# Performance work log

Measured on AMD Instinct MI355X. Metric: run time of the kernel, lower is better.

## Reference

```python
import jax, jax.numpy as jnp
import numpy as np

# Sparse grid constants (closed over; coords live on this grid)
B, H, W = 2, 640, 640
N = 409600
CIN, CH, COUT = 64, 64, 64
K = 3
PAD = (K - 1) // 2


def setup_inputs() -> dict:
    key = jax.random.key(0)
    ks = jax.random.split(key, 6)
    # unique active coordinates via permutation of the dense grid
    lin = jax.random.permutation(ks[0], B * H * W)[:N]
    b = lin // (H * W)
    rem = lin % (H * W)
    coords = jnp.stack([b, rem // W, rem % W], axis=1).astype(jnp.int32)  # [N,3]
    features = jax.random.normal(ks[1], (N, CIN), jnp.float32)
    w1 = jax.random.normal(ks[2], (K, K, CIN, CH), jnp.float32) * (1.0 / np.sqrt(K * K * CIN))
    b1 = jnp.zeros((CH,), jnp.float32)
    w2 = jax.random.normal(ks[3], (K, K, CH, COUT), jnp.float32) * (1.0 / np.sqrt(K * K * CH))
    b2 = jnp.zeros((COUT,), jnp.float32)
    wd = jax.random.normal(ks[4], (CIN, COUT), jnp.float32) * (1.0 / np.sqrt(CIN))
    return {"features": features, "coords": coords, "w1": w1, "b1": b1,
            "w2": w2, "b2": b2, "wd": wd}


def _build_grid(coords):
    # dense hash: grid[b,y,x] = row index into features, -1 if inactive
    grid = jnp.full((B, H, W), -1, dtype=jnp.int32)
    return grid.at[coords[:, 0], coords[:, 1], coords[:, 2]].set(
        jnp.arange(N, dtype=jnp.int32))


def _subm_conv(feat, coords, grid, w, bias):
    # Submanifold conv: out only at active sites; gather-matmul-accumulate per offset.
    cb, cy, cx = coords[:, 0], coords[:, 1], coords[:, 2]
    out = jnp.zeros((N, w.shape[-1]), feat.dtype)
    for ky in range(K):              # small fixed kernel loop (rulebook offsets)
        for kx in range(K):
            dy, dx = ky - PAD, kx - PAD
            ny, nx = cy + dy, cx + dx
            inb = (ny >= 0) & (ny < H) & (nx >= 0) & (nx < W)
            nidx = grid[cb, jnp.clip(ny, 0, H - 1), jnp.clip(nx, 0, W - 1)]
            valid = inb & (nidx >= 0)
            g = feat[jnp.where(valid, nidx, 0)]          # [N, Cin] gather
            g = jnp.where(valid[:, None], g, 0.0)
            out = out + g @ w[ky, kx]                    # per-offset GEMM
    if bias is not None:
        out = out + bias
    return out


def reference(features, coords, w1, b1, w2, b2, wd):
    grid = _build_grid(coords)
    out = jax.nn.relu(_subm_conv(features, coords, grid, w1, b1))
    out = jax.nn.relu(_subm_conv(out, coords, grid, w2, b2))
    residual = features @ wd                  # 1x1 subm conv, no bias
    out = jax.nn.relu(out + residual)         # sparse_add: identical index sets
    return out
```

## Files before the change

### kernel.cpp

```cpp
#include <hip/hip_runtime.h>
#include <hip/hip_bf16.h>
#include <stdint.h>

#define NP 409600
#define HG 640
#define WG 640
#define HW (HG*WG)
#define TPB  40
#define NTILE 3200

typedef __bf16 bf16x8 __attribute__((ext_vector_type(8)));
typedef float f32x4 __attribute__((ext_vector_type(4)));


__global__ void hist_kernel(const int* __restrict__ coords, int* __restrict__ hist,
                            int* __restrict__ grid) {
    int i = blockIdx.x * 256 + threadIdx.x;
    *(int2*)(grid + 2*i) = make_int2(-1, -1);
    int b = coords[3*i], y = coords[3*i+1], x = coords[3*i+2];
    atomicAdd(&hist[b*(TPB*TPB) + (y>>4)*TPB + (x>>4)], 1);
}

__global__ void scan_kernel(int* __restrict__ hist) {
    __shared__ int part[256];
    int t = threadIdx.x;
    int loc[13];
    int s = 0;
    #pragma unroll
    for (int k = 0; k < 13; ++k) {
        int idx = t*13 + k;
        int v = (idx < NTILE) ? hist[idx] : 0;
        loc[k] = s; s += v;
    }
    part[t] = s;
    __syncthreads();
    for (int off = 1; off < 256; off <<= 1) {
        int v = (t >= off) ? part[t - off] : 0;
        __syncthreads();
        part[t] += v;
        __syncthreads();
    }
    int pre = (t > 0) ? part[t-1] : 0;
    #pragma unroll
    for (int k = 0; k < 13; ++k) {
        int idx = t*13 + k;
        if (idx < NTILE) hist[idx] = pre + loc[k];
    }
}

__global__ void ord_kernel(const int* __restrict__ coords, int* __restrict__ offs,
                           int* __restrict__ ord, int* __restrict__ lsort,
                           int* __restrict__ grid, int* __restrict__ inv) {
    int i = blockIdx.x * 256 + threadIdx.x;
    int b = coords[3*i], y = coords[3*i+1], x = coords[3*i+2];
    int tile = b*(TPB*TPB) + (y>>4)*TPB + (x>>4);
    int pos = atomicAdd(&offs[tile], 1);
    int lin = b*HW + y*WG + x;
    ord[pos]   = i;
    lsort[pos] = lin;
    grid[lin]  = pos;
    inv[i]     = pos;
}

__global__ void perm_cast_kernel(const float* __restrict__ f, const int* __restrict__ inv,
                                 __hip_bfloat16* __restrict__ fpermb) {
    int t = blockIdx.x * 256 + threadIdx.x;
    int i = t >> 3, part = t & 7;
    int j = inv[i];
    const float4* p = (const float4*)(f + (long)i*64 + part*8);
    float4 a = p[0], b = p[1];
    union { uint4 q; __hip_bfloat16 h[8]; } u;
    u.h[0] = __float2bfloat16(a.x); u.h[1] = __float2bfloat16(a.y);
    u.h[2] = __float2bfloat16(a.z); u.h[3] = __float2bfloat16(a.w);
    u.h[4] = __float2bfloat16(b.x); u.h[5] = __float2bfloat16(b.y);
    u.h[6] = __float2bfloat16(b.z); u.h[7] = __float2bfloat16(b.w);
    *(uint4*)(fpermb + (long)j*64 + part*8) = u.q;
}

__global__ void nbr_kernel(const int* __restrict__ lsort, const int* __restrict__ grid,
                           int* __restrict__ nbrp) {
    int j = blockIdx.x * 256 + threadIdx.x;
    int lin = lsort[j];
    int b = lin / HW;
    int rem = lin - b*HW;
    int y = rem / WG;
    int x = rem - y*WG;
    int baseg = b*HW;
    #pragma unroll
    for (int tt = 0; tt < 9; ++tt) {
        if (tt == 4) continue;
        int ti = tt < 4 ? tt : tt - 1;
        int ny = y + tt/3 - 1, nx = x + tt%3 - 1;
        int g = -1;
        if (ny >= 0 && ny < HG && nx >= 0 && nx < WG)
            g = grid[baseg + ny*WG + nx];
        nbrp[ti*NP + j] = g;
    }
}

__global__ void cast_w_kernel(const float* __restrict__ w1, const float* __restrict__ w2,
                              const float* __restrict__ wd,
                              __hip_bfloat16* __restrict__ wc1, __hip_bfloat16* __restrict__ wc2) {
    int i = blockIdx.x * 256 + threadIdx.x;
    if (i < 9*4096) {
        int o = i;
        int e = o & 7, l = (o >> 3) & 63, c = (o >> 9) & 3, ks = (o >> 11) & 1, t = o >> 12;
        int n = c*16 + (l & 15), k = ks*32 + (l >> 4)*8 + e;
        wc1[o] = __float2bfloat16(w1[t*4096 + k*64 + n]);
    }
    int j = i - 9*4096;
    if (j >= 0 && j < 10*4096) {
        int o = j;
        int e = o & 7, l = (o >> 3) & 63, c = (o >> 9) & 3, ks = (o >> 11) & 1, t = o >> 12;
        int n = c*16 + (l & 15), k = ks*32 + (l >> 4)*8 + e;
        float v = (t < 9) ? w2[t*4096 + k*64 + n] : wd[k*64 + n];
        wc2[o] = __float2bfloat16(v);
    }
}


#define LDA 72

template<bool FINAL>
__launch_bounds__(256)
__global__ void conv_kernel(const __hip_bfloat16* __restrict__ src,
                            const __hip_bfloat16* __restrict__ idsrc,
                            const int* __restrict__ nbrp,
                            const int* __restrict__ ord,
                            const __hip_bfloat16* __restrict__ wT,
                            const float* __restrict__ bias,
                            __hip_bfloat16* __restrict__ out_bf,
                            float* __restrict__ out_f) {
    __shared__ __align__(16) __hip_bfloat16 As[2][128 * LDA];

    const int tid = threadIdx.x;
    const int sbid = (blockIdx.x & 7) * 400 + (blockIdx.x >> 3);
    const int base = sbid * 128;
    const int wave = tid >> 6, lane = tid & 63;
    const int mrow = lane & 15, kq = lane >> 4;
    const int srow = tid >> 1, shalf = tid & 1;

    const bf16x8* wfrag = (const bf16x8*)wT;

    f32x4 acc[2][4];
    #pragma unroll
    for (int i = 0; i < 2; ++i)
        #pragma unroll
        for (int j = 0; j < 4; ++j)
            acc[i][j] = (f32x4){0.f, 0.f, 0.f, 0.f};

    auto gpos = [&](int t) -> int {
        if (t == 4) return base + srow;
        int ti = t < 4 ? t : t - 1;
        return nbrp[ti*NP + base + srow];
    };

    auto stageA = [&](int g, int bsel) {
        uint4 v0, v1, v2, v3;
        if (g >= 0) {
            const uint4* p = (const uint4*)(src + (long)g*64 + shalf*32);
            v0 = p[0]; v1 = p[1]; v2 = p[2]; v3 = p[3];
        } else {
            v0 = v1 = v2 = v3 = make_uint4(0u, 0u, 0u, 0u);
        }
        uint4* dst = (uint4*)(As[bsel] + srow*LDA + shalf*32);
        dst[0] = v0; dst[1] = v1; dst[2] = v2; dst[3] = v3;
    };

    auto mfma_tap = [&](f32x4 (&ac)[2][4], int t, int cur) {
        #pragma unroll
        for (int ks = 0; ks < 2; ++ks) {
            int kb = ks*32 + kq*8;
            bf16x8 a0 = *(const bf16x8*)(&As[cur][(wave*32      + mrow)*LDA + kb]);
            bf16x8 a1 = *(const bf16x8*)(&As[cur][(wave*32 + 16 + mrow)*LDA + kb]);
            int fb = ((t*2 + ks)*4)*64 + lane;
            bf16x8 b0 = wfrag[fb];
            bf16x8 b1 = wfrag[fb + 64];
            bf16x8 b2 = wfrag[fb + 128];
            bf16x8 b3 = wfrag[fb + 192];
            ac[0][0] = __builtin_amdgcn_mfma_f32_16x16x32_bf16(a0, b0, ac[0][0], 0, 0, 0);
            ac[0][1] = __builtin_amdgcn_mfma_f32_16x16x32_bf16(a0, b1, ac[0][1], 0, 0, 0);
            ac[0][2] = __builtin_amdgcn_mfma_f32_16x16x32_bf16(a0, b2, ac[0][2], 0, 0, 0);
            ac[0][3] = __builtin_amdgcn_mfma_f32_16x16x32_bf16(a0, b3, ac[0][3], 0, 0, 0);
            ac[1][0] = __builtin_amdgcn_mfma_f32_16x16x32_bf16(a1, b0, ac[1][0], 0, 0, 0);
            ac[1][1] = __builtin_amdgcn_mfma_f32_16x16x32_bf16(a1, b1, ac[1][1], 0, 0, 0);
            ac[1][2] = __builtin_amdgcn_mfma_f32_16x16x32_bf16(a1, b2, ac[1][2], 0, 0, 0);
            ac[1][3] = __builtin_amdgcn_mfma_f32_16x16x32_bf16(a1, b3, ac[1][3], 0, 0, 0);
        }
    };

    int g = gpos(0);
    stageA(g, 0);
    g = gpos(1);

    for (int t = 0; t < 9; ++t) {
        __syncthreads();
        if (t + 1 < 9) {
            stageA(g, (t + 1) & 1);
            if (t + 2 < 9) g = gpos(t + 2);
        }
        mfma_tap(acc, t, t & 1);
    }

    const int col = mrow, quad = kq;

    if (FINAL) {
        f32x4 accR[2][4];
        #pragma unroll
        for (int i = 0; i < 2; ++i)
            #pragma unroll
            for (int j = 0; j < 4; ++j)
                accR[i][j] = (f32x4){0.f, 0.f, 0.f, 0.f};
        const int r0 = base + wave*32 + mrow, r1 = r0 + 16;
        #pragma unroll
        for (int ks = 0; ks < 2; ++ks) {
            int kb = ks*32 + kq*8;
            union { uint4 q; bf16x8 v; } ua0, ua1;
            ua0.q = *(const uint4*)(idsrc + (long)r0*64 + kb);
            ua1.q = *(const uint4*)(idsrc + (long)r1*64 + kb);
            int fb = ((9*2 + ks)*4)*64 + lane;
            bf16x8 b0 = wfrag[fb];
            bf16x8 b1 = wfrag[fb + 64];
            bf16x8 b2 = wfrag[fb + 128];
            bf16x8 b3 = wfrag[fb + 192];
            accR[0][0] = __builtin_amdgcn_mfma_f32_16x16x32_bf16(ua0.v, b0, accR[0][0], 0, 0, 0);
            accR[0][1] = __builtin_amdgcn_mfma_f32_16x16x32_bf16(ua0.v, b1, accR[0][1], 0, 0, 0);
            accR[0][2] = __builtin_amdgcn_mfma_f32_16x16x32_bf16(ua0.v, b2, accR[0][2], 0, 0, 0);
            accR[0][3] = __builtin_amdgcn_mfma_f32_16x16x32_bf16(ua0.v, b3, accR[0][3], 0, 0, 0);
            accR[1][0] = __builtin_amdgcn_mfma_f32_16x16x32_bf16(ua1.v, b0, accR[1][0], 0, 0, 0);
            accR[1][1] = __builtin_amdgcn_mfma_f32_16x16x32_bf16(ua1.v, b1, accR[1][1], 0, 0, 0);
            accR[1][2] = __builtin_amdgcn_mfma_f32_16x16x32_bf16(ua1.v, b2, accR[1][2], 0, 0, 0);
            accR[1][3] = __builtin_amdgcn_mfma_f32_16x16x32_bf16(ua1.v, b3, accR[1][3], 0, 0, 0);
        }
        #pragma unroll
        for (int cb = 0; cb < 4; ++cb) {
            float bv = bias[cb*16 + col];
            #pragma unroll
            for (int mb = 0; mb < 2; ++mb) {
                #pragma unroll
                for (int r = 0; r < 4; ++r) {
                    float v = acc[mb][cb][r] + bv;
                    v = v > 0.f ? v : 0.f;
                    v += accR[mb][cb][r];
                    v = v > 0.f ? v : 0.f;
                    int srt = base + wave*32 + mb*16 + quad*4 + r;
                    long row = ord[srt];
                    out_f[row*64 + cb*16 + col] = v;
                }
            }
        }
    } else {
        #pragma unroll
        for (int cb = 0; cb < 4; ++cb) {
            float bv = bias[cb*16 + col];
            #pragma unroll
            for (int mb = 0; mb < 2; ++mb) {
                #pragma unroll
                for (int r = 0; r < 4; ++r) {
                    float v = acc[mb][cb][r] + bv;
                    v = v > 0.f ? v : 0.f;
                    int srt = base + wave*32 + mb*16 + quad*4 + r;
                    out_bf[(long)srt*64 + cb*16 + col] = __float2bfloat16(v);
                }
            }
        }
    }
}


extern "C" void kernel_launch(void* const* d_in, const int* in_sizes, int n_in,
                              void* d_out, int out_size, void* d_ws, size_t ws_size,
                              hipStream_t stream) {
    const float* features = (const float*)d_in[0];
    const int*   coords   = (const int*)d_in[1];
    const float* w1 = (const float*)d_in[2];
    const float* b1 = (const float*)d_in[3];
    const float* w2 = (const float*)d_in[4];
    const float* b2 = (const float*)d_in[5];
    const float* wd = (const float*)d_in[6];
    float* out = (float*)d_out;

    char* ws = (char*)d_ws;
    int*            grid   = (int*)ws;
    int*            nbrp   = (int*)(ws + 3276800);
    int*            ord    = (int*)(ws + 16384000);
    __hip_bfloat16* fpermb = (__hip_bfloat16*)(ws + 18022400);
    __hip_bfloat16* y1     = (__hip_bfloat16*)(ws + 70451200);
    __hip_bfloat16* wc1    = (__hip_bfloat16*)(ws + 122880000);
    __hip_bfloat16* wc2    = (__hip_bfloat16*)(ws + 122953728);
    int* lsort = (int*)(ws + 70451200);
    int* hist  = (int*)(ws + 70451200 + 1638400);
    int* inv   = (int*)(ws + 70451200 + 1651200);

    hipMemsetAsync(hist, 0x00, (size_t)NTILE * sizeof(int), stream);

    hist_kernel     <<<1600,  256, 0, stream>>>(coords, hist, grid);
    scan_kernel     <<<1,     256, 0, stream>>>(hist);
    ord_kernel      <<<1600,  256, 0, stream>>>(coords, hist, ord, lsort, grid, inv);
    cast_w_kernel   <<<304,   256, 0, stream>>>(w1, w2, wd, wc1, wc2);
    nbr_kernel      <<<1600,  256, 0, stream>>>(lsort, grid, nbrp);
    perm_cast_kernel<<<12800, 256, 0, stream>>>(features, inv, fpermb);

    conv_kernel<false><<<3200, 256, 0, stream>>>(fpermb, nullptr, nbrp, ord, wc1, b1, y1, nullptr);
    conv_kernel<true ><<<3200, 256, 0, stream>>>(y1, fpermb, nbrp, ord, wc2, b2, nullptr, out);
}
```

Baseline: 419.1 us.

## Make conv gather wave-private to drop block barriers, add MFMA priority

Each wave now gathers its own 32 rows into a private single-buffered LDS tile instead of the block cooperatively filling a shared double-buffered 128-row tile. This removes the per-tap __syncthreads and cuts LDS use. The invalid-neighbour branch becomes a branchless clamp-and-mask, and the MFMA section is raised with s_setprio. The trade-off is less cross-tap prefetch overlap within a wave: there is a single LDS buffer, and only the neighbour index is prefetched one tap ahead, which relies on occupancy and compiler scheduling to hide gather latency.

Measured after the change: 431.3 us. +2.9%, slower.

```diff
diff --git a/kernel.cpp b/kernel.cpp
--- a/kernel.cpp
+++ b/kernel.cpp
@@ -131,15 +131,17 @@
                             const float* __restrict__ bias,
                             __hip_bfloat16* __restrict__ out_bf,
                             float* __restrict__ out_f) {
-    __shared__ __align__(16) __hip_bfloat16 As[2][128 * LDA];
+    __shared__ __align__(16) __hip_bfloat16 As[4][32 * LDA];
 
     const int tid = threadIdx.x;
     const int sbid = (blockIdx.x & 7) * 400 + (blockIdx.x >> 3);
     const int base = sbid * 128;
     const int wave = tid >> 6, lane = tid & 63;
     const int mrow = lane & 15, kq = lane >> 4;
-    const int srow = tid >> 1, shalf = tid & 1;
-
+    const int wrow = lane >> 1, h = lane & 1;
+    const int grow = base + wave*32 + wrow;
+
+    __hip_bfloat16* Aw = As[wave];
     const bf16x8* wfrag = (const bf16x8*)wT;
 
     f32x4 acc[2][4];
@@ -150,56 +152,48 @@
             acc[i][j] = (f32x4){0.f, 0.f, 0.f, 0.f};
 
     auto gpos = [&](int t) -> int {
-        if (t == 4) return base + srow;
+        if (t == 4) return grow;
         int ti = t < 4 ? t : t - 1;
-        return nbrp[ti*NP + base + srow];
+        return nbrp[ti*NP + grow];
     };
 
-    auto stageA = [&](int g, int bsel) {
-        uint4 v0, v1, v2, v3;
-        if (g >= 0) {
-            const uint4* p = (const uint4*)(src + (long)g*64 + shalf*32);
-            v0 = p[0]; v1 = p[1]; v2 = p[2]; v3 = p[3];
-        } else {
-            v0 = v1 = v2 = v3 = make_uint4(0u, 0u, 0u, 0u);
-        }
-        uint4* dst = (uint4*)(As[bsel] + srow*LDA + shalf*32);
+    int gv = gpos(0);
+
+    #pragma unroll
+    for (int t = 0; t < 9; ++t) {
+        int  gc = gv < 0 ? 0 : gv;
+        uint vm = gv < 0 ? 0u : ~0u;
+        const uint4* p = (const uint4*)(src + (long)gc*64 + h*32);
+        uint4 v0 = p[0], v1 = p[1], v2 = p[2], v3 = p[3];
+        if (t + 1 < 9) gv = gpos(t + 1);
+        v0.x &= vm; v0.y &= vm; v0.z &= vm; v0.w &= vm;
+        v1.x &= vm; v1.y &= vm; v1.z &= vm; v1.w &= vm;
+        v2.x &= vm; v2.y &= vm; v2.z &= vm; v2.w &= vm;
+        v3.x &= vm; v3.y &= vm; v3.z &= vm; v3.w &= vm;
+        uint4* dst = (uint4*)(Aw + wrow*LDA + h*32);
         dst[0] = v0; dst[1] = v1; dst[2] = v2; dst[3] = v3;
-    };
-
-    auto mfma_tap = [&](f32x4 (&ac)[2][4], int t, int cur) {
+
+        __builtin_amdgcn_s_setprio(1);
         #pragma unroll
         for (int ks = 0; ks < 2; ++ks) {
             int kb = ks*32 + kq*8;
-            bf16x8 a0 = *(const bf16x8*)(&As[cur][(wave*32      + mrow)*LDA + kb]);
-            bf16x8 a1 = *(const bf16x8*)(&As[cur][(wave*32 + 16 + mrow)*LDA + kb]);
+            bf16x8 a0 = *(const bf16x8*)(Aw + (     mrow)*LDA + kb);
+            bf16x8 a1 = *(const bf16x8*)(Aw + (16 + mrow)*LDA + kb);
             int fb = ((t*2 + ks)*4)*64 + lane;
             bf16x8 b0 = wfrag[fb];
             bf16x8 b1 = wfrag[fb + 64];
             bf16x8 b2 = wfrag[fb + 128];
             bf16x8 b3 = wfrag[fb + 192];
-            ac[0][0] = __builtin_amdgcn_mfma_f32_16x16x32_bf16(a0, b0, ac[0][0], 0, 0, 0);
-            ac[0][1] = __builtin_amdgcn_mfma_f32_16x16x32_bf16(a0, b1, ac[0][1], 0, 0, 0);
-            ac[0][2] = __builtin_amdgcn_mfma_f32_16x16x32_bf16(a0, b2, ac[0][2], 0, 0, 0);
-            ac[0][3] = __builtin_amdgcn_mfma_f32_16x16x32_bf16(a0, b3, ac[0][3], 0, 0, 0);
-            ac[1][0] = __builtin_amdgcn_mfma_f32_16x16x32_bf16(a1, b0, ac[1][0], 0, 0, 0);
-            ac[1][1] = __builtin_amdgcn_mfma_f32_16x16x32_bf16(a1, b1, ac[1][1], 0, 0, 0);
-            ac[1][2] = __builtin_amdgcn_mfma_f32_16x16x32_bf16(a1, b2, ac[1][2], 0, 0, 0);
-            ac[1][3] = __builtin_amdgcn_mfma_f32_16x16x32_bf16(a1, b3, ac[1][3], 0, 0, 0);
+            acc[0][0] = __builtin_amdgcn_mfma_f32_16x16x32_bf16(a0, b0, acc[0][0], 0, 0, 0);
+            acc[0][1] = __builtin_amdgcn_mfma_f32_16x16x32_bf16(a0, b1, acc[0][1], 0, 0, 0);
+            acc[0][2] = __builtin_amdgcn_mfma_f32_16x16x32_bf16(a0, b2, acc[0][2], 0, 0, 0);
+            acc[0][3] = __builtin_amdgcn_mfma_f32_16x16x32_bf16(a0, b3, acc[0][3], 0, 0, 0);
+            acc[1][0] = __builtin_amdgcn_mfma_f32_16x16x32_bf16(a1, b0, acc[1][0], 0, 0, 0);
+            acc[1][1] = __builtin_amdgcn_mfma_f32_16x16x32_bf16(a1, b1, acc[1][1], 0, 0, 0);
+            acc[1][2] = __builtin_amdgcn_mfma_f32_16x16x32_bf16(a1, b2, acc[1][2], 0, 0, 0);
+            acc[1][3] = __builtin_amdgcn_mfma_f32_16x16x32_bf16(a1, b3, acc[1][3], 0, 0, 0);
         }
-    };
-
-    int g = gpos(0);
-    stageA(g, 0);
-    g = gpos(1);
-
-    for (int t = 0; t < 9; ++t) {
-        __syncthreads();
-        if (t + 1 < 9) {
-            stageA(g, (t + 1) & 1);
-            if (t + 2 < 9) g = gpos(t + 2);
-        }
-        mfma_tap(acc, t, t & 1);
+        __builtin_amdgcn_s_setprio(0);
     }
 
     const int col = mrow, quad = kq;
```
